# Kernel optimization log

Hardware: AMD Instinct MI355X
Metric: run time of the kernel (lower is better)

The kernel has to match this reference:

```python
import jax, jax.numpy as jnp
import numpy as np

N, E, D_IN, D_OUT = 50000, 800000, 128, 128


def setup_inputs() -> dict:
    key = jax.random.key(0)
    ks = jax.random.split(key, 4)
    x = jax.random.normal(ks[0], (N, D_IN), jnp.float32)
    edge_index = jax.random.randint(ks[1], (2, E), 0, N)
    # GCNConv.lin weight (no bias in lin; bias added after aggregation)
    W = jax.random.normal(ks[2], (D_IN, D_OUT), jnp.float32) / np.sqrt(D_IN)
    b = jnp.zeros((D_OUT,), jnp.float32)
    # edge_weight_predictor: Linear(2*dim_in, 1)
    w_pred = jax.random.normal(ks[3], (2 * D_IN, 1), jnp.float32) / np.sqrt(2 * D_IN)
    b_pred = jnp.zeros((1,), jnp.float32)
    return {"x": x, "edge_index": edge_index, "W": W, "b": b,
            "w_pred": w_pred, "b_pred": b_pred}


def reference(x, edge_index, W, b, w_pred, b_pred):
    n = x.shape[0]
    src, tgt = edge_index[0], edge_index[1]

    # --- learned edge weights: gather, concat, linear, sigmoid ---
    eemb = jnp.concatenate([x[src], x[tgt]], axis=1)          # [E, 2D]
    ew = jax.nn.sigmoid(eemb @ w_pred + b_pred)[:, 0]         # [E]

    # --- GCNConv with edge_weight (PyG gcn_norm: add self-loops w=1) ---
    loop = jnp.arange(n)
    row = jnp.concatenate([src, loop])                        # message sources
    col = jnp.concatenate([tgt, loop])                        # aggregation targets
    w_full = jnp.concatenate([ew, jnp.ones((n,), ew.dtype)])

    deg = jax.ops.segment_sum(w_full, col, num_segments=n)    # weighted in-degree
    dis = jnp.where(deg > 0, jax.lax.rsqrt(deg), 0.0)         # deg^{-1/2}, inf->0
    norm = dis[row] * w_full * dis[col]                       # [E+N]

    xw = x @ W                                                # [N, D_OUT]
    msg = norm[:, None] * xw[row]                             # [E+N, D_OUT]
    out = jax.ops.segment_sum(msg, col, num_segments=n) + b   # [N, D_OUT]
    return out
```

## Files before the change

### kernel.cpp

```cpp
#include <hip/hip_runtime.h>
#include <math.h>

#define D 128
#define NC 16

typedef __attribute__((ext_vector_type(8))) short bf16x8;
typedef __attribute__((ext_vector_type(4))) float f32x4;

__device__ __forceinline__ unsigned int bf16_round(float f) {
  unsigned int u = __float_as_uint(f);
  return (u + 0x7fffu + ((u >> 16) & 1u)) >> 16;
}
__device__ __forceinline__ float bf_lo(unsigned int u) { return __uint_as_float(u << 16); }
__device__ __forceinline__ float bf_hi(unsigned int u) { return __uint_as_float(u & 0xffff0000u); }

__global__ __launch_bounds__(256) void k_pq(const float* __restrict__ x,
                                            const float* __restrict__ w_pred,
                                            const float* __restrict__ W,
                                            float* __restrict__ p, float* __restrict__ q,
                                            unsigned int* __restrict__ xbh,
                                            unsigned short* __restrict__ wt,
                                            int* __restrict__ partial, int n) {
  int tid = blockIdx.x * 256 + threadIdx.x;
  int total = NC * n;
  int gsz = gridDim.x * 256;
  for (int i = tid; i < total; i += gsz) partial[i] = 0;
  if (tid < 16384) {
    int col = tid >> 7, k = tid & 127;
    wt[col * 128 + k] = (unsigned short)bf16_round(W[k * 128 + col]);
  }
  int wid = tid >> 6;
  int lane = threadIdx.x & 63;
  if (wid >= n) return;
  float2 xv = ((const float2*)(x + (size_t)wid * D))[lane];
  xbh[(size_t)wid * 64 + lane] = bf16_round(xv.x) | (bf16_round(xv.y) << 16);
  float2 wp = ((const float2*)w_pred)[lane];
  float2 wq = ((const float2*)w_pred)[64 + lane];
  float pp = xv.x * wp.x + xv.y * wp.y;
  float qq = xv.x * wq.x + xv.y * wq.y;
#pragma unroll
  for (int off = 32; off > 0; off >>= 1) {
    pp += __shfl_down(pp, off);
    qq += __shfl_down(qq, off);
  }
  if (lane == 0) { p[wid] = pp; q[wid] = qq; }
}

__global__ __launch_bounds__(256) void k_hist(const int* __restrict__ tgt,
                                              int* __restrict__ rank,
                                              int* __restrict__ partial,
                                              int E, int n) {
  int e = blockIdx.x * blockDim.x + threadIdx.x;
  if (e >= E) return;
  int t = tgt[e];
  int c = (e >> 8) & (NC - 1);
  rank[e] = atomicAdd(&partial[c * n + t], 1);
}

__global__ __launch_bounds__(256) void k_scan1(const int* __restrict__ partial,
                                               int* __restrict__ rowptr,
                                               int* __restrict__ bsum, int n) {
  __shared__ int wsum[4];
  int base = blockIdx.x * 1024 + threadIdx.x * 4;
  int4 v = make_int4(0, 0, 0, 0);
  if (base + 3 < n) {
#pragma unroll
    for (int c = 0; c < NC; ++c) {
      int4 t = *(const int4*)(partial + (size_t)c * n + base);
      v.x += t.x; v.y += t.y; v.z += t.z; v.w += t.w;
    }
  } else {
#pragma unroll
    for (int c = 0; c < NC; ++c) {
      const int* pc = partial + (size_t)c * n;
      if (base + 0 < n) v.x += pc[base + 0];
      if (base + 1 < n) v.y += pc[base + 1];
      if (base + 2 < n) v.z += pc[base + 2];
      if (base + 3 < n) v.w += pc[base + 3];
    }
  }
  int s = v.x + v.y + v.z + v.w;
  int lane = threadIdx.x & 63;
  int wave = threadIdx.x >> 6;
  int incl = s;
#pragma unroll
  for (int off = 1; off < 64; off <<= 1) {
    int t = __shfl_up(incl, off);
    if (lane >= off) incl += t;
  }
  if (lane == 63) wsum[wave] = incl;
  __syncthreads();
  int woff = 0;
#pragma unroll
  for (int w = 0; w < 4; ++w) if (w < wave) woff += wsum[w];
  int excl = woff + incl - s;
  if (base + 0 < n) rowptr[base + 0] = excl;
  if (base + 1 < n) rowptr[base + 1] = excl + v.x;
  if (base + 2 < n) rowptr[base + 2] = excl + v.x + v.y;
  if (base + 3 < n) rowptr[base + 3] = excl + v.x + v.y + v.z;
  if (threadIdx.x == 255) bsum[blockIdx.x] = woff + incl;
}

__global__ __launch_bounds__(256) void k_cursors(int* __restrict__ rowptr,
                                                 const int* __restrict__ bsum,
                                                 const int* __restrict__ partial,
                                                 int* __restrict__ cursor,
                                                 int n, int E, int nb) {
  __shared__ int bpre_s[64];
  if (threadIdx.x < 64) {
    int lane = threadIdx.x;
    int v = (lane < nb) ? bsum[lane] : 0;
    int incl = v;
#pragma unroll
    for (int off = 1; off < 64; off <<= 1) {
      int t = __shfl_up(incl, off);
      if (lane >= off) incl += t;
    }
    bpre_s[lane] = incl - v;
  }
  __syncthreads();
  int t = blockIdx.x * blockDim.x + threadIdx.x;
  if (t < n) {
    int r = rowptr[t] + bpre_s[t >> 10];
    rowptr[t] = r;
#pragma unroll
    for (int c = 0; c < NC; ++c) {
      cursor[c * n + t] = r;
      r += partial[c * n + t];
    }
  }
  if (t == 0) rowptr[n] = E;
}

__global__ __launch_bounds__(256) void k_fill(const int* __restrict__ src,
                                              const int* __restrict__ tgt,
                                              const int* __restrict__ rank,
                                              const int* __restrict__ cursor,
                                              const float* __restrict__ p,
                                              const float* __restrict__ q,
                                              const float* __restrict__ b_pred,
                                              int2* __restrict__ epair, int E, int n) {
  int e = blockIdx.x * blockDim.x + threadIdx.x;
  if (e >= E) return;
  int s = src[e], t = tgt[e];
  int c = (e >> 8) & (NC - 1);
  int pos = cursor[c * n + t] + rank[e];
  float z = p[s] + q[t] + b_pred[0];
  float w = 1.0f / (1.0f + expf(-z));
  epair[pos] = make_int2(s, __float_as_int(w));
}

__global__ __launch_bounds__(256) void k_dis(const int* __restrict__ rowptr,
                                             const int2* __restrict__ epair,
                                             float* __restrict__ dis, int n) {
  int wid = (blockIdx.x * blockDim.x + threadIdx.x) >> 6;
  int lane = threadIdx.x & 63;
  if (wid >= n) return;
  int beg = rowptr[wid], end = rowptr[wid + 1];
  float sum = 0.0f;
  for (int j = beg + lane; j < end; j += 64) sum += __int_as_float(epair[j].y);
#pragma unroll
  for (int off = 32; off > 0; off >>= 1) sum += __shfl_down(sum, off);
  if (lane == 0) {
    float d = 1.0f + sum;
    dis[wid] = (d > 0.0f) ? rsqrtf(d) : 0.0f;
  }
}

__global__ __launch_bounds__(256) void k_gemm_mfma(const short* __restrict__ xbh,
                                                   const short* __restrict__ wt,
                                                   const float* __restrict__ dis,
                                                   unsigned int* __restrict__ xwh, int n) {
  __shared__ float cbuf[4][16 * 128];
  int wave = threadIdx.x >> 6;
  int lane = threadIdx.x & 63;
  int row0 = blockIdx.x * 64 + wave * 16;
  int rA = lane & 15, quad = lane >> 4;

  f32x4 acc[8];
#pragma unroll
  for (int cb = 0; cb < 8; ++cb) acc[cb] = (f32x4){0.f, 0.f, 0.f, 0.f};

  const short* arow = xbh + (size_t)(row0 + rA) * 128 + quad * 8;
  bool arow_ok = (row0 + rA) < n;
#pragma unroll
  for (int kk = 0; kk < 4; ++kk) {
    bf16x8 a;
    if (arow_ok) a = *(const bf16x8*)(arow + kk * 32);
    else a = (bf16x8){0, 0, 0, 0, 0, 0, 0, 0};
#pragma unroll
    for (int cb = 0; cb < 8; ++cb) {
      bf16x8 bf = *(const bf16x8*)(wt + (size_t)(cb * 16 + rA) * 128 + kk * 32 + quad * 8);
      acc[cb] = __builtin_amdgcn_mfma_f32_16x16x32_bf16(a, bf, acc[cb], 0, 0, 0);
    }
  }

#pragma unroll
  for (int cb = 0; cb < 8; ++cb)
#pragma unroll
    for (int r = 0; r < 4; ++r)
      cbuf[wave][(quad * 4 + r) * 128 + cb * 16 + rA] = acc[cb][r];
  __syncthreads();

  int rr = lane >> 2;
  int ch = (lane & 3) * 32;
  int grow = row0 + rr;
  if (grow < n) {
    float dv = dis[grow];
    const float* cr = &cbuf[wave][rr * 128 + ch];
#pragma unroll
    for (int g = 0; g < 2; ++g) {
      uint4 o;
      o.x = bf16_round(cr[g * 16 + 0] * dv)  | (bf16_round(cr[g * 16 + 1] * dv) << 16);
      o.y = bf16_round(cr[g * 16 + 2] * dv)  | (bf16_round(cr[g * 16 + 3] * dv) << 16);
      o.z = bf16_round(cr[g * 16 + 4] * dv)  | (bf16_round(cr[g * 16 + 5] * dv) << 16);
      o.w = bf16_round(cr[g * 16 + 6] * dv)  | (bf16_round(cr[g * 16 + 7] * dv) << 16);
      uint4 o2;
      o2.x = bf16_round(cr[g * 16 + 8] * dv)  | (bf16_round(cr[g * 16 + 9] * dv) << 16);
      o2.y = bf16_round(cr[g * 16 + 10] * dv) | (bf16_round(cr[g * 16 + 11] * dv) << 16);
      o2.z = bf16_round(cr[g * 16 + 12] * dv) | (bf16_round(cr[g * 16 + 13] * dv) << 16);
      o2.w = bf16_round(cr[g * 16 + 14] * dv) | (bf16_round(cr[g * 16 + 15] * dv) << 16);
      *(uint4*)(xwh + (size_t)grow * 64 + (ch >> 1) + g * 8)     = o;
      *(uint4*)(xwh + (size_t)grow * 64 + (ch >> 1) + g * 8 + 4) = o2;
    }
  }
}

__global__ __launch_bounds__(256) void k_gather(const int* __restrict__ rowptr,
                                                const int2* __restrict__ epair,
                                                const uint4* __restrict__ xwh4,
                                                const float* __restrict__ dis,
                                                const float* __restrict__ b,
                                                float* __restrict__ out, int n) {
  int wid = (blockIdx.x * blockDim.x + threadIdx.x) >> 6;
  int lane = threadIdx.x & 63;
  if (wid >= n) return;
  int cj = lane & 15;
  int rg = lane >> 4;
  int beg = rowptr[wid], end = rowptr[wid + 1];

  float acc[8];
  if (rg == 0) {
    uint4 v = xwh4[(size_t)wid * 16 + cj];
    acc[0] = bf_lo(v.x); acc[1] = bf_hi(v.x);
    acc[2] = bf_lo(v.y); acc[3] = bf_hi(v.y);
    acc[4] = bf_lo(v.z); acc[5] = bf_hi(v.z);
    acc[6] = bf_lo(v.w); acc[7] = bf_hi(v.w);
  } else {
#pragma unroll
    for (int i = 0; i < 8; ++i) acc[i] = 0.0f;
  }

  for (int j0 = beg; j0 < end; j0 += 64) {
    int m = end - j0; if (m > 64) m = 64;
    int sl = 0; float cl = 0.0f;
    if (lane < m) {
      int2 pr = epair[j0 + lane];
      sl = pr.x; cl = __int_as_float(pr.y);
    }
    for (int k = 0; k < m; k += 4) {
      int idx = k + rg;
      int s = __shfl(sl, idx);
      float c = __shfl(cl, idx);
      if (idx >= m) { s = 0; c = 0.0f; }
      uint4 v = xwh4[(size_t)s * 16 + cj];
      acc[0] = fmaf(c, bf_lo(v.x), acc[0]);
      acc[1] = fmaf(c, bf_hi(v.x), acc[1]);
      acc[2] = fmaf(c, bf_lo(v.y), acc[2]);
      acc[3] = fmaf(c, bf_hi(v.y), acc[3]);
      acc[4] = fmaf(c, bf_lo(v.z), acc[4]);
      acc[5] = fmaf(c, bf_hi(v.z), acc[5]);
      acc[6] = fmaf(c, bf_lo(v.w), acc[6]);
      acc[7] = fmaf(c, bf_hi(v.w), acc[7]);
    }
  }

#pragma unroll
  for (int i = 0; i < 8; ++i) {
    acc[i] += __shfl_xor(acc[i], 16);
    acc[i] += __shfl_xor(acc[i], 32);
  }

  if (rg == 0) {
    float dt = dis[wid];
    float4 b0 = ((const float4*)b)[cj * 2];
    float4 b1 = ((const float4*)b)[cj * 2 + 1];
    float4 o0, o1;
    o0.x = fmaf(dt, acc[0], b0.x); o0.y = fmaf(dt, acc[1], b0.y);
    o0.z = fmaf(dt, acc[2], b0.z); o0.w = fmaf(dt, acc[3], b0.w);
    o1.x = fmaf(dt, acc[4], b1.x); o1.y = fmaf(dt, acc[5], b1.y);
    o1.z = fmaf(dt, acc[6], b1.z); o1.w = fmaf(dt, acc[7], b1.w);
    ((float4*)out)[(size_t)wid * 32 + cj * 2] = o0;
    ((float4*)out)[(size_t)wid * 32 + cj * 2 + 1] = o1;
  }
}

extern "C" void kernel_launch(void* const* d_in, const int* in_sizes, int n_in,
                              void* d_out, int out_size, void* d_ws, size_t ws_size,
                              hipStream_t stream) {
  const float* x      = (const float*)d_in[0];
  const int*   ei     = (const int*)d_in[1];
  const float* W      = (const float*)d_in[2];
  const float* b      = (const float*)d_in[3];
  const float* w_pred = (const float*)d_in[4];
  const float* b_pred = (const float*)d_in[5];

  int n = in_sizes[0] / D;
  int E = in_sizes[1] / 2;
  const int* src = ei;
  const int* tgt = ei + E;

  float* out = (float*)d_out;
  float* ws  = (float*)d_ws;
  unsigned int* xwh = (unsigned int*)ws;
  unsigned int* xbh = xwh + (size_t)n * 64;
  float* p       = (float*)(xbh + (size_t)n * 64);
  float* q       = p + n;
  float* dis     = q + n;
  int2*  epair   = (int2*)(dis + n);
  int*   rank    = (int*)(epair + E);
  int*   partial = rank + E;
  int*   cursor  = partial + (size_t)NC * n;
  int*   rowptr  = cursor + (size_t)NC * n;
  int*   bsum    = rowptr + n + 1;
  unsigned short* wt = (unsigned short*)(bsum + 64);

  int nb = (n + 1023) / 1024;

  k_pq<<<(n + 3) / 4, 256, 0, stream>>>(x, w_pred, W, p, q, xbh, wt, partial, n);
  k_hist<<<(E + 255) / 256, 256, 0, stream>>>(tgt, rank, partial, E, n);
  k_scan1<<<nb, 256, 0, stream>>>(partial, rowptr, bsum, n);
  k_cursors<<<(n + 255) / 256, 256, 0, stream>>>(rowptr, bsum, partial, cursor, n, E, nb);
  k_fill<<<(E + 255) / 256, 256, 0, stream>>>(src, tgt, rank, cursor, p, q, b_pred, epair, E, n);
  k_dis<<<(n + 3) / 4, 256, 0, stream>>>(rowptr, epair, dis, n);
  k_gemm_mfma<<<(n + 63) / 64, 256, 0, stream>>>((const short*)xbh, (const short*)wt, dis, xwh, n);
  k_gather<<<(n + 3) / 4, 256, 0, stream>>>(rowptr, epair, (const uint4*)xwh, dis, b, out, n);
}
```

Measured before the change: 209.9 us.

## Fuse histogram into preprocessing kernel and degree computation into GEMM

Merges the edge histogram pass into the x-preprocessing kernel by interleaving histogram blocks with per-node blocks in one launch, and moves zeroing of the partial counters to a memset. The separate degree kernel is removed: the GEMM kernel now sums each row's edge weights with four lanes per row before the MFMA loop and writes dis. The number of histogram chunks is doubled to cut atomic contention, which doubles the size of the partial/cursor arrays that the scan kernels read. The goal is fewer launches and less per-kernel overhead.

```diff
diff --git a/kernel.cpp b/kernel.cpp
--- a/kernel.cpp
+++ b/kernel.cpp
@@ -2,7 +2,7 @@
 #include <math.h>
 
 #define D 128
-#define NC 16
+#define NC 32
 
 typedef __attribute__((ext_vector_type(8))) short bf16x8;
 typedef __attribute__((ext_vector_type(4))) float f32x4;
@@ -14,22 +14,35 @@
 __device__ __forceinline__ float bf_lo(unsigned int u) { return __uint_as_float(u << 16); }
 __device__ __forceinline__ float bf_hi(unsigned int u) { return __uint_as_float(u & 0xffff0000u); }
 
-__global__ __launch_bounds__(256) void k_pq(const float* __restrict__ x,
-                                            const float* __restrict__ w_pred,
-                                            const float* __restrict__ W,
-                                            float* __restrict__ p, float* __restrict__ q,
-                                            unsigned int* __restrict__ xbh,
-                                            unsigned short* __restrict__ wt,
-                                            int* __restrict__ partial, int n) {
-  int tid = blockIdx.x * 256 + threadIdx.x;
-  int total = NC * n;
-  int gsz = gridDim.x * 256;
-  for (int i = tid; i < total; i += gsz) partial[i] = 0;
-  if (tid < 16384) {
-    int col = tid >> 7, k = tid & 127;
+__global__ __launch_bounds__(256) void k_pre(const float* __restrict__ x,
+                                             const float* __restrict__ w_pred,
+                                             const float* __restrict__ W,
+                                             const int* __restrict__ tgt,
+                                             float* __restrict__ p, float* __restrict__ q,
+                                             unsigned int* __restrict__ xbh,
+                                             unsigned short* __restrict__ wt,
+                                             int* __restrict__ rank,
+                                             int* __restrict__ partial,
+                                             int n, int E, int nbHist, int total) {
+  int bid = blockIdx.x;
+  long long h0 = (long long)bid * nbHist / total;
+  long long h1 = (long long)(bid + 1) * nbHist / total;
+  if (h1 != h0) {
+    int e = (int)h0 * 256 + threadIdx.x;
+    if (e < E) {
+      int t = tgt[e];
+      int c = (e >> 8) & (NC - 1);
+      rank[e] = atomicAdd(&partial[c * n + t], 1);
+    }
+    return;
+  }
+  int pqIdx = bid - (int)h1;
+  int ptid = pqIdx * 256 + threadIdx.x;
+  if (ptid < 16384) {
+    int col = ptid >> 7, k = ptid & 127;
     wt[col * 128 + k] = (unsigned short)bf16_round(W[k * 128 + col]);
   }
-  int wid = tid >> 6;
+  int wid = ptid >> 6;
   int lane = threadIdx.x & 63;
   if (wid >= n) return;
   float2 xv = ((const float2*)(x + (size_t)wid * D))[lane];
@@ -44,17 +57,6 @@
     qq += __shfl_down(qq, off);
   }
   if (lane == 0) { p[wid] = pp; q[wid] = qq; }
-}
-
-__global__ __launch_bounds__(256) void k_hist(const int* __restrict__ tgt,
-                                              int* __restrict__ rank,
-                                              int* __restrict__ partial,
-                                              int E, int n) {
-  int e = blockIdx.x * blockDim.x + threadIdx.x;
-  if (e >= E) return;
-  int t = tgt[e];
-  int c = (e >> 8) & (NC - 1);
-  rank[e] = atomicAdd(&partial[c * n + t], 1);
 }
 
 __global__ __launch_bounds__(256) void k_scan1(const int* __restrict__ partial,
@@ -150,33 +152,32 @@
   epair[pos] = make_int2(s, __float_as_int(w));
 }
 
-__global__ __launch_bounds__(256) void k_dis(const int* __restrict__ rowptr,
-                                             const int2* __restrict__ epair,
-                                             float* __restrict__ dis, int n) {
-  int wid = (blockIdx.x * blockDim.x + threadIdx.x) >> 6;
-  int lane = threadIdx.x & 63;
-  if (wid >= n) return;
-  int beg = rowptr[wid], end = rowptr[wid + 1];
-  float sum = 0.0f;
-  for (int j = beg + lane; j < end; j += 64) sum += __int_as_float(epair[j].y);
-#pragma unroll
-  for (int off = 32; off > 0; off >>= 1) sum += __shfl_down(sum, off);
-  if (lane == 0) {
-    float d = 1.0f + sum;
-    dis[wid] = (d > 0.0f) ? rsqrtf(d) : 0.0f;
-  }
-}
-
 __global__ __launch_bounds__(256) void k_gemm_mfma(const short* __restrict__ xbh,
                                                    const short* __restrict__ wt,
-                                                   const float* __restrict__ dis,
+                                                   const int* __restrict__ rowptr,
+                                                   const int2* __restrict__ epair,
+                                                   float* __restrict__ dis,
                                                    unsigned int* __restrict__ xwh, int n) {
   __shared__ float cbuf[4][16 * 128];
   int wave = threadIdx.x >> 6;
   int lane = threadIdx.x & 63;
   int row0 = blockIdx.x * 64 + wave * 16;
+
+  int rr = lane >> 2, jj = lane & 3;
+  int grow = row0 + rr;
+  float dv = 0.0f;
+  if (grow < n) {
+    int beg = rowptr[grow], end = rowptr[grow + 1];
+    float sum = 0.0f;
+    for (int j = beg + jj; j < end; j += 4) sum += __int_as_float(epair[j].y);
+    sum += __shfl_xor(sum, 1);
+    sum += __shfl_xor(sum, 2);
+    float d = 1.0f + sum;
+    dv = (d > 0.0f) ? rsqrtf(d) : 0.0f;
+    if (jj == 0) dis[grow] = dv;
+  }
+
   int rA = lane & 15, quad = lane >> 4;
-
   f32x4 acc[8];
 #pragma unroll
   for (int cb = 0; cb < 8; ++cb) acc[cb] = (f32x4){0.f, 0.f, 0.f, 0.f};
@@ -202,11 +203,8 @@
       cbuf[wave][(quad * 4 + r) * 128 + cb * 16 + rA] = acc[cb][r];
   __syncthreads();
 
-  int rr = lane >> 2;
-  int ch = (lane & 3) * 32;
-  int grow = row0 + rr;
+  int ch = jj * 32;
   if (grow < n) {
-    float dv = dis[grow];
     const float* cr = &cbuf[wave][rr * 128 + ch];
 #pragma unroll
     for (int g = 0; g < 2; ++g) {
@@ -326,13 +324,17 @@
   unsigned short* wt = (unsigned short*)(bsum + 64);
 
   int nb = (n + 1023) / 1024;
-
-  k_pq<<<(n + 3) / 4, 256, 0, stream>>>(x, w_pred, W, p, q, xbh, wt, partial, n);
-  k_hist<<<(E + 255) / 256, 256, 0, stream>>>(tgt, rank, partial, E, n);
+  int nbPq = (n + 3) / 4;
+  int nbHist = (E + 255) / 256;
+  int total = nbPq + nbHist;
+
+  (void)hipMemsetAsync(partial, 0, (size_t)NC * n * sizeof(int), stream);
+  k_pre<<<total, 256, 0, stream>>>(x, w_pred, W, tgt, p, q, xbh, wt, rank, partial,
+                                   n, E, nbHist, total);
   k_scan1<<<nb, 256, 0, stream>>>(partial, rowptr, bsum, n);
   k_cursors<<<(n + 255) / 256, 256, 0, stream>>>(rowptr, bsum, partial, cursor, n, E, nb);
   k_fill<<<(E + 255) / 256, 256, 0, stream>>>(src, tgt, rank, cursor, p, q, b_pred, epair, E, n);
-  k_dis<<<(n + 3) / 4, 256, 0, stream>>>(rowptr, epair, dis, n);
-  k_gemm_mfma<<<(n + 63) / 64, 256, 0, stream>>>((const short*)xbh, (const short*)wt, dis, xwh, n);
+  k_gemm_mfma<<<(n + 63) / 64, 256, 0, stream>>>((const short*)xbh, (const short*)wt,
+                                                 rowptr, epair, dis, xwh, n);
   k_gather<<<(n + 3) / 4, 256, 0, stream>>>(rowptr, epair, (const uint4*)xwh, dis, b, out, n);
 }
```

Result: faster. 198.1 us (-5.6%).
